# Performance work log

Hardware: AMD Instinct MI355X
Metric: run time of the kernel (lower is better)

## Reference

```python
import jax, jax.numpy as jnp
import numpy as np

K = 20
EPS = 1e-5


def knn_idx(x, k):
    # x: (B, N, C) -> (B, N, k) indices of k nearest neighbors (incl. self)
    xx = jnp.sum(x * x, axis=-1, keepdims=True)           # (B,N,1)
    inner = -2.0 * jnp.einsum('bnc,bmc->bnm', x, x)        # (B,N,N)
    pd = -xx - inner - jnp.swapaxes(xx, 1, 2)              # negative sq dist
    _, idx = jax.lax.top_k(pd, k)                          # (B,N,k)
    return idx


def get_graph_feature(x, k=K):
    B, N, C = x.shape
    idx = knn_idx(x, k)                                    # (B,N,k)
    # gather neighbor features per batch
    feature = jax.vmap(lambda xb, ib: xb[ib])(x, idx)      # (B,N,k,C)
    xe = jnp.broadcast_to(x[:, :, None, :], (B, N, k, C))  # (B,N,k,C)
    f = jnp.concatenate([feature - xe, xe], axis=3)        # (B,N,k,2C)
    return jnp.transpose(f, (0, 3, 1, 2))                  # (B,2C,N,k)


def conv1x1(x, W, b):
    # x: (B,Cin,N,k), W: (Cout,Cin)
    return jnp.einsum('bcnk,oc->bonk', x, W) + b[None, :, None, None]


def batchnorm(x, gamma, beta):
    # training-mode BN over (B,N,k) per channel, biased variance (torch default)
    mean = jnp.mean(x, axis=(0, 2, 3), keepdims=True)
    var = jnp.var(x, axis=(0, 2, 3), keepdims=True)
    xhat = (x - mean) * jax.lax.rsqrt(var + EPS)
    return xhat * gamma[None, :, None, None] + beta[None, :, None, None]


def setup_inputs() -> dict:
    key = jax.random.key(0)
    ks = jax.random.split(key, 10)
    B, N, C = 4, 4096, 3
    x = jax.random.normal(ks[0], (B, N, C), dtype=jnp.float32)
    W1 = jax.random.normal(ks[1], (64, 2 * C), dtype=jnp.float32) * 0.1
    b1 = jnp.zeros((64,), jnp.float32)
    g1 = jnp.ones((64,), jnp.float32)
    be1 = jnp.zeros((64,), jnp.float32)
    W2 = jax.random.normal(ks[2], (128, 64), dtype=jnp.float32) * 0.1
    b2 = jnp.zeros((128,), jnp.float32)
    g2 = jnp.ones((128,), jnp.float32)
    be2 = jnp.zeros((128,), jnp.float32)
    W3 = jax.random.normal(ks[3], (128, 128), dtype=jnp.float32) * 0.1
    b3 = jnp.zeros((128,), jnp.float32)
    g3 = jnp.ones((128,), jnp.float32)
    be3 = jnp.zeros((128,), jnp.float32)
    return {"x": x, "W1": W1, "b1": b1, "g1": g1, "be1": be1,
            "W2": W2, "b2": b2, "g2": g2, "be2": be2,
            "W3": W3, "b3": b3, "g3": g3, "be3": be3}


def reference(x, W1, b1, g1, be1, W2, b2, g2, be2, W3, b3, g3, be3):
    f = get_graph_feature(x, K)                  # (B,6,N,k)
    h = jax.nn.relu(batchnorm(conv1x1(f, W1, b1), g1, be1))
    h = jax.nn.relu(batchnorm(conv1x1(h, W2, b2), g2, be2))
    h = batchnorm(conv1x1(h, W3, b3), g3, be3)
    return jnp.max(h, axis=-1)                   # (B,128,N)
```

## Files before the change

kernel.cpp:

```cpp
#include <hip/hip_runtime.h>


typedef __attribute__((ext_vector_type(8)))  short short8;
typedef __attribute__((ext_vector_type(4)))  float floatx4;

#define BATCH 4
#define NPTS  4096
#define KNN   20
#define BN_   (BATCH*NPTS)
#define CNT   (BATCH*NPTS*KNN)

__device__ __forceinline__ unsigned short f2bf(float f) {
  unsigned u = __float_as_uint(f);
  unsigned r = u + 0x7FFFu + ((u >> 16) & 1u);
  return (unsigned short)(r >> 16);
}

__device__ __forceinline__ unsigned cvtpk(float lo, float hi) {
  unsigned r;
  asm("v_cvt_pk_bf16_f32 %0, %1, %2" : "=v"(r) : "v"(lo), "v"(hi));
  return r;
}

union PK8 { unsigned u4[4]; short8 s; };

__device__ __forceinline__ void store4bf_relu(unsigned short* dst, floatx4 v) {
  unsigned lo = cvtpk(fmaxf(v[0],0.f), fmaxf(v[1],0.f));
  unsigned hi = cvtpk(fmaxf(v[2],0.f), fmaxf(v[3],0.f));
  *(uint2*)dst = make_uint2(lo, hi);
}

__device__ __forceinline__ unsigned mono(float f) {
  unsigned u = __float_as_uint(f);
  return u ^ ((unsigned)((int)u >> 31) | 0x80000000u);
}

__device__ __forceinline__ void bn_affine(float gsum, float gsq, float gamma,
                                          float beta, float& s, float& sh) {
  const float inv = 1.0f / (float)CNT;
  float mean = gsum * inv;
  float var  = gsq * inv - mean * mean;
  s  = gamma * rsqrtf(var + 1e-5f);
  sh = beta - mean * s;
}

__global__ void pf_prep(const float* __restrict__ x, float4* __restrict__ xp,
                        float* __restrict__ stats,
                        const float* __restrict__ W2, const float* __restrict__ W3,
                        unsigned short* __restrict__ w2p,
                        unsigned short* __restrict__ w3p) {
  int pt = blockIdx.x * 256 + threadIdx.x;
  float x0 = x[pt*3+0], x1 = x[pt*3+1], x2 = x[pt*3+2];
  float xx = x0*x0 + x1*x1 + x2*x2;
  xp[pt] = make_float4(x0, x1, x2, xx);
  if (blockIdx.x == 0)
    for (int i = threadIdx.x; i < 640; i += 256) stats[i] = 0.0f;
  if (blockIdx.x == 1) {
    for (int i = threadIdx.x; i < 128*64;  i += 256) w2p[i] = f2bf(W2[i]);
    for (int i = threadIdx.x; i < 128*128; i += 256) w3p[i] = f2bf(W3[i]);
  }
}

__device__ __forceinline__ float sort_take20th(float v, int lane) {
  #pragma unroll
  for (int k = 2; k <= 64; k <<= 1) {
    #pragma unroll
    for (int j = k >> 1; j >= 1; j >>= 1) {
      float o = __shfl_xor(v, j);
      bool keepmax = (((lane & j) == 0) == ((lane & k) == 0));
      v = keepmax ? fmaxf(v, o) : fminf(v, o);
    }
  }
  return __shfl(v, 19);
}

__device__ __forceinline__ unsigned long long sort64_desc(unsigned long long v,
                                                          int lane) {
  #pragma unroll
  for (int k = 2; k <= 64; k <<= 1) {
    #pragma unroll
    for (int j = k >> 1; j >= 1; j >>= 1) {
      unsigned long long o = __shfl_xor(v, j);
      bool keepmax = (((lane & j) == 0) == ((lane & k) == 0));
      unsigned long long hi = v > o ? v : o;
      unsigned long long lo = v > o ? o : v;
      v = keepmax ? hi : lo;
    }
  }
  return v;
}

__global__ __launch_bounds__(256) void pf_knn(const float4* __restrict__ xp,
                                              int* __restrict__ idxb) {
  __shared__ unsigned long long lst[16][128];
  __shared__ int lcnt[16];
  const int tid  = threadIdx.x;
  const int lane = tid & 63;
  const int w    = tid >> 6;
  const int b    = blockIdx.x >> 8;
  const int nb   = (blockIdx.x & 255) * 16 + w * 4;
  const float4* xb = xp + b * NPTS;

  float4 q0 = xb[nb], q1 = xb[nb+1], q2 = xb[nb+2], q3 = xb[nb+3];

  float mx0=-3.0e38f, mx1=-3.0e38f, mx2=-3.0e38f, mx3=-3.0e38f;
  for (int j0 = 0; j0 < NPTS; j0 += 64) {
    float4 c = xb[j0 + lane];
    float d0 = fmaf(q0.x,c.x, fmaf(q0.y,c.y, q0.z*c.z));
    float d1 = fmaf(q1.x,c.x, fmaf(q1.y,c.y, q1.z*c.z));
    float d2 = fmaf(q2.x,c.x, fmaf(q2.y,c.y, q2.z*c.z));
    float d3 = fmaf(q3.x,c.x, fmaf(q3.y,c.y, q3.z*c.z));
    mx0 = fmaxf(mx0, fmaf(2.f,d0,-q0.w) - c.w);
    mx1 = fmaxf(mx1, fmaf(2.f,d1,-q1.w) - c.w);
    mx2 = fmaxf(mx2, fmaf(2.f,d2,-q2.w) - c.w);
    mx3 = fmaxf(mx3, fmaf(2.f,d3,-q3.w) - c.w);
  }
  float T0 = sort_take20th(mx0, lane);
  float T1 = sort_take20th(mx1, lane);
  float T2 = sort_take20th(mx2, lane);
  float T3 = sort_take20th(mx3, lane);

  if (lane < 4) lcnt[w*4 + lane] = 0;
  __syncthreads();

  for (int j0 = 0; j0 < NPTS; j0 += 64) {
    float4 c = xb[j0 + lane];
    float d0 = fmaf(q0.x,c.x, fmaf(q0.y,c.y, q0.z*c.z));
    float d1 = fmaf(q1.x,c.x, fmaf(q1.y,c.y, q1.z*c.z));
    float d2 = fmaf(q2.x,c.x, fmaf(q2.y,c.y, q2.z*c.z));
    float d3 = fmaf(q3.x,c.x, fmaf(q3.y,c.y, q3.z*c.z));
    float p0 = fmaf(2.f,d0,-q0.w) - c.w;
    float p1 = fmaf(2.f,d1,-q1.w) - c.w;
    float p2 = fmaf(2.f,d2,-q2.w) - c.w;
    float p3 = fmaf(2.f,d3,-q3.w) - c.w;
    unsigned long long keybase = (unsigned long long)(4095 - (j0 + lane));
    if (p0 >= T0) {
      int o = atomicAdd(&lcnt[w*4+0], 1);
      if (o < 128) lst[w*4+0][o] = ((unsigned long long)mono(p0) << 32) | keybase;
    }
    if (p1 >= T1) {
      int o = atomicAdd(&lcnt[w*4+1], 1);
      if (o < 128) lst[w*4+1][o] = ((unsigned long long)mono(p1) << 32) | keybase;
    }
    if (p2 >= T2) {
      int o = atomicAdd(&lcnt[w*4+2], 1);
      if (o < 128) lst[w*4+2][o] = ((unsigned long long)mono(p2) << 32) | keybase;
    }
    if (p3 >= T3) {
      int o = atomicAdd(&lcnt[w*4+3], 1);
      if (o < 128) lst[w*4+3][o] = ((unsigned long long)mono(p3) << 32) | keybase;
    }
  }

  #pragma unroll 1
  for (int i = 0; i < 4; ++i) {
    const int li = w*4 + i;
    const int cn = lcnt[li];
    const int outbase = (b * NPTS + nb + i) * KNN;
    if (cn <= 64) {
      unsigned long long v = (lane < cn) ? lst[li][lane] : 0ull;
      v = sort64_desc(v, lane);
      if (lane < KNN) idxb[outbase + lane] = 4095 - (int)(v & 0xFFFFFFFFull);
    } else if (cn <= 128) {
      unsigned long long e0 = lst[li][lane];
      unsigned long long e1 = (lane + 64 < cn) ? lst[li][lane + 64] : 0ull;
      #pragma unroll 1
      for (int r = 0; r < KNN; ++r) {
        unsigned long long m = e0 > e1 ? e0 : e1;
        #pragma unroll
        for (int o = 32; o; o >>= 1) {
          unsigned long long t = __shfl_xor(m, o);
          m = t > m ? t : m;
        }
        if (lane == 0) idxb[outbase + r] = 4095 - (int)(m & 0xFFFFFFFFull);
        if (e0 == m) e0 = 0ull; else if (e1 == m) e1 = 0ull;
      }
    } else {
      const float4 qq = (i == 0) ? q0 : (i == 1) ? q1 : (i == 2) ? q2 : q3;
      unsigned long long prev = ~0ull;
      #pragma unroll 1
      for (int r = 0; r < KNN; ++r) {
        unsigned long long best = 0ull;
        for (int j0 = 0; j0 < NPTS; j0 += 64) {
          float4 c = xb[j0 + lane];
          float dd = fmaf(qq.x,c.x, fmaf(qq.y,c.y, qq.z*c.z));
          float pd = fmaf(2.f,dd,-qq.w) - c.w;
          unsigned long long key = ((unsigned long long)mono(pd) << 32) |
                                   (unsigned long long)(4095 - (j0 + lane));
          if (key < prev && key > best) best = key;
        }
        #pragma unroll
        for (int o = 32; o; o >>= 1) {
          unsigned long long t = __shfl_xor(best, o);
          best = t > best ? t : best;
        }
        if (lane == 0) idxb[outbase + r] = 4095 - (int)(best & 0xFFFFFFFFull);
        prev = best;
      }
    }
  }
}

__global__ __launch_bounds__(256) void pf_mom(
    const float4* __restrict__ xp, const int* __restrict__ idxb,
    float* __restrict__ gm) {
  __shared__ float WM[4][27];
  const int tid = threadIdx.x, lane = tid & 63, w = tid >> 6;
  const int pt = blockIdx.x * 256 + tid;
  const float4 xi = xp[pt];
  const int ib = (pt >> 12) << 12;

  int idx[KNN];
  const int4* ip = (const int4*)(idxb + pt*KNN);
  #pragma unroll
  for (int q = 0; q < 5; ++q) {
    int4 v = ip[q];
    idx[q*4+0]=v.x; idx[q*4+1]=v.y; idx[q*4+2]=v.z; idx[q*4+3]=v.w;
  }
  float sj0=0,sj1=0,sj2=0, p0=0,p1=0,p2=0,p3=0,p4=0,p5=0;
  #pragma unroll
  for (int kk = 0; kk < KNN; ++kk) {
    float4 xj = xp[ib + idx[kk]];
    sj0 += xj.x; sj1 += xj.y; sj2 += xj.z;
    p0 = fmaf(xj.x,xj.x,p0); p1 = fmaf(xj.x,xj.y,p1); p2 = fmaf(xj.x,xj.z,p2);
    p3 = fmaf(xj.y,xj.y,p3); p4 = fmaf(xj.y,xj.z,p4); p5 = fmaf(xj.z,xj.z,p5);
  }
  float m[27];
  m[0]=sj0; m[1]=sj1; m[2]=sj2;
  m[3]=20.f*xi.x; m[4]=20.f*xi.y; m[5]=20.f*xi.z;
  m[6]=p0; m[7]=p1; m[8]=p2; m[9]=p3; m[10]=p4; m[11]=p5;
  m[12]=20.f*xi.x*xi.x; m[13]=20.f*xi.x*xi.y; m[14]=20.f*xi.x*xi.z;
  m[15]=20.f*xi.y*xi.y; m[16]=20.f*xi.y*xi.z; m[17]=20.f*xi.z*xi.z;
  m[18]=sj0*xi.x; m[19]=sj0*xi.y; m[20]=sj0*xi.z;
  m[21]=sj1*xi.x; m[22]=sj1*xi.y; m[23]=sj1*xi.z;
  m[24]=sj2*xi.x; m[25]=sj2*xi.y; m[26]=sj2*xi.z;
  #pragma unroll
  for (int c = 0; c < 27; ++c) {
    float v = m[c];
    #pragma unroll
    for (int o = 32; o; o >>= 1) v += __shfl_xor(v, o);
    m[c] = v;
  }
  if (lane == 0)
    #pragma unroll
    for (int c = 0; c < 27; ++c) WM[w][c] = m[c];
  __syncthreads();
  if (tid < 27) atomicAdd(&gm[tid], WM[0][tid]+WM[1][tid]+WM[2][tid]+WM[3][tid]);
}

__global__ void pf_affine1(const float* __restrict__ gm,
                           const float* __restrict__ W1,
                           const float* __restrict__ g1,
                           const float* __restrict__ be1,
                           unsigned short* __restrict__ w1s,
                           float* __restrict__ sh1e) {
  int c = threadIdx.x;
  if (c >= 64) return;
  const float* wr = W1 + c*6;
  const float wa[3] = {wr[0], wr[1], wr[2]};
  const float wb[3] = {wr[3], wr[4], wr[5]};
  const int si0[9] = {0,1,2, 1,3,4, 2,4,5};
  float syf = 0.f, sy2 = 0.f;
  #pragma unroll
  for (int a = 0; a < 3; ++a)
    syf += wa[a]*(gm[a] - gm[3+a]) + wb[a]*gm[3+a];
  #pragma unroll
  for (int a = 0; a < 3; ++a)
    #pragma unroll
    for (int bq = 0; bq < 3; ++bq) {
      int k = a*3 + bq, kt = bq*3 + a;
      float pjj = gm[6 + si0[k]], pii = gm[12 + si0[k]];
      float cc = gm[18 + k], ct = gm[18 + kt];
      float uu = pjj - cc - ct + pii;
      float uv = cc - pii;
      sy2 += wa[a]*wa[bq]*uu + 2.f*wa[a]*wb[bq]*uv + wb[a]*wb[bq]*pii;
    }
  const float inv = 1.0f / (float)CNT;
  float mean = syf * inv;
  float var  = sy2 * inv - mean * mean;
  float s  = g1[c] * rsqrtf(var + 1e-5f);
  sh1e[c]  = be1[c] - mean * s;
  unsigned short* o = w1s + c*8;
  o[0]=f2bf(s*wa[0]); o[1]=f2bf(s*wa[1]); o[2]=f2bf(s*wa[2]);
  o[3]=f2bf(s*wb[0]); o[4]=f2bf(s*wb[1]); o[5]=f2bf(s*wb[2]);
  o[6]=0; o[7]=0;
}

__global__ void pf_affine2(const float* __restrict__ gs2,
                           const float* __restrict__ gq2,
                           const float* __restrict__ W2,
                           const float* __restrict__ g2,
                           const float* __restrict__ be2,
                           unsigned short* __restrict__ w2s,
                           float* __restrict__ shm2) {
  int c = threadIdx.x;
  if (c >= 128) return;
  float s, sh; bn_affine(gs2[c], gq2[c], g2[c], be2[c], s, sh);
  shm2[c] = sh;
  const float* wr = W2 + c*64;
  unsigned short* o = w2s + c*64;
  for (int j = 0; j < 64; ++j) o[j] = f2bf(s * wr[j]);
}

__global__ __launch_bounds__(256, 4) void pf_stats2(
    const float4* __restrict__ xp, const int* __restrict__ idxb,
    const unsigned short* __restrict__ w1s, const float* __restrict__ sh1e,
    const unsigned short* __restrict__ w2p,
    float* __restrict__ gs2, float* __restrict__ gq2) {
  __shared__ __align__(16) short8 AF[KNN][16];
  __shared__ __align__(16) unsigned short H1[2][16][72];
  __shared__ float SS[128], SQ[128];

  const int tid = threadIdx.x;
  const int lane = tid & 63, ww = tid >> 6;
  const int l15 = lane & 15, quad = lane >> 4;
  const int pt0 = blockIdx.x * 16;

  if (tid < 128) { SS[tid] = 0.f; SQ[tid] = 0.f; }

  for (int u = tid; u < 16*KNN; u += 256) {
    int kk = u >> 4, pp = u & 15;
    int pt = pt0 + pp;
    float4 xi = xp[pt];
    float4 xj = xp[((pt >> 12) << 12) + idxb[pt*KNN + kk]];
    PK8 U;
    U.u4[0] = cvtpk(xj.x-xi.x, xj.y-xi.y);
    U.u4[1] = cvtpk(xj.z-xi.z, xi.x);
    U.u4[2] = cvtpk(xi.y, xi.z);
    U.u4[3] = 0;
    AF[kk][pp] = U.s;
  }

  short8 w1f = *(const short8*)(w1s + (16*ww + l15)*8);
  floatx4 sh1v;
  #pragma unroll
  for (int r = 0; r < 4; ++r) sh1v[r] = sh1e[16*ww + 4*quad + r];

  short8 w2f[2][2];
  #pragma unroll
  for (int ks = 0; ks < 2; ++ks)
    #pragma unroll
    for (int t = 0; t < 2; ++t)
      w2f[ks][t] = *(const short8*)(w2p + (32*ww + 16*t + l15)*64 + 32*ks + quad*8);

  float sum[2][4] = {{0,0,0,0},{0,0,0,0}}, sq[2][4] = {{0,0,0,0},{0,0,0,0}};
  const short8 z8 = {0,0,0,0,0,0,0,0};
  __syncthreads();

  #pragma unroll 1
  for (int kk = 0; kk < KNN; ++kk) {
    short8 a0 = z8;
    if (quad == 0) a0 = AF[kk][l15];
    floatx4 c0 = sh1v;
    c0 = __builtin_amdgcn_mfma_f32_16x16x32_bf16(w1f, a0, c0, 0,0,0);
    store4bf_relu(&H1[kk & 1][l15][16*ww + 4*quad], c0);
    __syncthreads();
    floatx4 acc2[2] = {{0,0,0,0},{0,0,0,0}};
    #pragma unroll
    for (int ks = 0; ks < 2; ++ks) {
      short8 a = *(const short8*)&H1[kk & 1][l15][ks*32 + quad*8];
      #pragma unroll
      for (int t = 0; t < 2; ++t)
        acc2[t] = __builtin_amdgcn_mfma_f32_16x16x32_bf16(w2f[ks][t], a, acc2[t], 0,0,0);
    }
    #pragma unroll
    for (int t = 0; t < 2; ++t)
      #pragma unroll
      for (int r = 0; r < 4; ++r) {
        float v = acc2[t][r];
        sum[t][r] += v; sq[t][r] = fmaf(v, v, sq[t][r]);
      }
  }
  #pragma unroll
  for (int t = 0; t < 2; ++t)
    #pragma unroll
    for (int r = 0; r < 4; ++r) {
      float s = sum[t][r], z = sq[t][r];
      s += __shfl_xor(s, 1); z += __shfl_xor(z, 1);
      s += __shfl_xor(s, 2); z += __shfl_xor(z, 2);
      s += __shfl_xor(s, 4); z += __shfl_xor(z, 4);
      s += __shfl_xor(s, 8); z += __shfl_xor(z, 8);
      if (l15 == 0) {
        int ch = 32*ww + 16*t + 4*quad + r;
        atomicAdd(&SS[ch], s); atomicAdd(&SQ[ch], z);
      }
    }
  __syncthreads();
  if (tid < 128) { atomicAdd(&gs2[tid], SS[tid]); atomicAdd(&gq2[tid], SQ[tid]); }
}

__global__ __launch_bounds__(256, 4) void pf_main(
    const float4* __restrict__ xp, const int* __restrict__ idxb,
    const unsigned short* __restrict__ w1s, const float* __restrict__ sh1e,
    const unsigned short* __restrict__ w2s, const float* __restrict__ shm2,
    const unsigned short* __restrict__ w3p,
    float* __restrict__ gs3, float* __restrict__ gq3,
    float* __restrict__ maxv) {
  __shared__ __align__(16) short8 AF[KNN][16];
  __shared__ __align__(16) unsigned short H1[16][72];
  __shared__ __align__(16) unsigned short H2[16][136];
  __shared__ float SS[128], SQ[128];

  const int tid = threadIdx.x;
  const int lane = tid & 63, ww = tid >> 6;
  const int l15 = lane & 15, quad = lane >> 4;
  const int pt0 = blockIdx.x * 16;

  if (tid < 128) { SS[tid] = 0.f; SQ[tid] = 0.f; }

  for (int u = tid; u < 16*KNN; u += 256) {
    int kk = u >> 4, pp = u & 15;
    int pt = pt0 + pp;
    float4 xi = xp[pt];
    float4 xj = xp[((pt >> 12) << 12) + idxb[pt*KNN + kk]];
    PK8 U;
    U.u4[0] = cvtpk(xj.x-xi.x, xj.y-xi.y);
    U.u4[1] = cvtpk(xj.z-xi.z, xi.x);
    U.u4[2] = cvtpk(xi.y, xi.z);
    U.u4[3] = 0;
    AF[kk][pp] = U.s;
  }

  short8 w1f = *(const short8*)(w1s + (16*ww + l15)*8);
  floatx4 sh1v;
  #pragma unroll
  for (int r = 0; r < 4; ++r) sh1v[r] = sh1e[16*ww + 4*quad + r];
  short8 w2f[2][2];
  #pragma unroll
  for (int ks = 0; ks < 2; ++ks)
    #pragma unroll
    for (int t = 0; t < 2; ++t)
      w2f[ks][t] = *(const short8*)(w2s + (32*ww + 16*t + l15)*64 + 32*ks + quad*8);
  floatx4 sh2v[2];
  #pragma unroll
  for (int t = 0; t < 2; ++t)
    #pragma unroll
    for (int r = 0; r < 4; ++r)
      sh2v[t][r] = shm2[32*ww + 16*t + 4*quad + r];
  short8 w3f[4][2];
  #pragma unroll
  for (int ks = 0; ks < 4; ++ks)
    #pragma unroll
    for (int t = 0; t < 2; ++t)
      w3f[ks][t] = *(const short8*)(w3p + (32*ww + 16*t + l15)*128 + 32*ks + quad*8);

  float sum[2][4] = {{0,0,0,0},{0,0,0,0}}, sq[2][4] = {{0,0,0,0},{0,0,0,0}};
  float mx[2][4];
  #pragma unroll
  for (int t = 0; t < 2; ++t)
    #pragma unroll
    for (int r = 0; r < 4; ++r) mx[t][r] = -3.0e38f;

  const short8 z8 = {0,0,0,0,0,0,0,0};
  __syncthreads();

  #pragma unroll 1
  for (int kk = 0; kk < KNN; ++kk) {
    short8 a0 = z8;
    if (quad == 0) a0 = AF[kk][l15];
    floatx4 acc1 = sh1v;
    acc1 = __builtin_amdgcn_mfma_f32_16x16x32_bf16(w1f, a0, acc1, 0,0,0);
    store4bf_relu(&H1[l15][16*ww + 4*quad], acc1);
    __syncthreads();
    floatx4 acc2[2] = {sh2v[0], sh2v[1]};
    #pragma unroll
    for (int ks = 0; ks < 2; ++ks) {
      short8 a = *(const short8*)&H1[l15][ks*32 + quad*8];
      #pragma unroll
      for (int t = 0; t < 2; ++t)
        acc2[t] = __builtin_amdgcn_mfma_f32_16x16x32_bf16(w2f[ks][t], a, acc2[t], 0,0,0);
    }
    #pragma unroll
    for (int t = 0; t < 2; ++t)
      store4bf_relu(&H2[l15][32*ww + 16*t + 4*quad], acc2[t]);
    __syncthreads();
    floatx4 acc3[2] = {{0,0,0,0},{0,0,0,0}};
    #pragma unroll
    for (int ks = 0; ks < 4; ++ks) {
      short8 a = *(const short8*)&H2[l15][ks*32 + quad*8];
      #pragma unroll
      for (int t = 0; t < 2; ++t)
        acc3[t] = __builtin_amdgcn_mfma_f32_16x16x32_bf16(w3f[ks][t], a, acc3[t], 0,0,0);
    }
    #pragma unroll
    for (int t = 0; t < 2; ++t)
      #pragma unroll
      for (int r = 0; r < 4; ++r) {
        float v = acc3[t][r];
        sum[t][r] += v; sq[t][r] = fmaf(v, v, sq[t][r]);
        mx[t][r] = fmaxf(mx[t][r], v);
      }
  }

  #pragma unroll
  for (int t = 0; t < 2; ++t) {
    int ch0 = 32*ww + 16*t + 4*quad;
    float4 o = make_float4(mx[t][0], mx[t][1], mx[t][2], mx[t][3]);
    *(float4*)&maxv[(size_t)(pt0 + l15)*128 + ch0] = o;
  }
  #pragma unroll
  for (int t = 0; t < 2; ++t)
    #pragma unroll
    for (int r = 0; r < 4; ++r) {
      float s = sum[t][r], z = sq[t][r];
      s += __shfl_xor(s, 1); z += __shfl_xor(z, 1);
      s += __shfl_xor(s, 2); z += __shfl_xor(z, 2);
      s += __shfl_xor(s, 4); z += __shfl_xor(z, 4);
      s += __shfl_xor(s, 8); z += __shfl_xor(z, 8);
      if (l15 == 0) {
        int ch = 32*ww + 16*t + 4*quad + r;
        atomicAdd(&SS[ch], s); atomicAdd(&SQ[ch], z);
      }
    }
  __syncthreads();
  if (tid < 128) { atomicAdd(&gs3[tid], SS[tid]); atomicAdd(&gq3[tid], SQ[tid]); }
}

__global__ __launch_bounds__(256) void pf_out(
    const float* __restrict__ maxv,
    const float* __restrict__ gs3, const float* __restrict__ gq3,
    const float* __restrict__ g3, const float* __restrict__ be3,
    float* __restrict__ out) {
  __shared__ float T[128][17];
  __shared__ float SC[128], SH[128];
  const int tid = threadIdx.x;
  const int b  = blockIdx.x >> 8;
  const int n0 = (blockIdx.x & 255) * 16;
  if (tid < 128) {
    float s, sh; bn_affine(gs3[tid], gq3[tid], g3[tid], be3[tid], s, sh);
    SC[tid] = s; SH[tid] = sh;
  }
  __syncthreads();
  const float4* mv4 = (const float4*)maxv;
  #pragma unroll
  for (int r = 0; r < 2; ++r) {
    int fid = r * 256 + tid;
    int nl = fid >> 5, c4 = fid & 31;
    float4 v = mv4[(size_t)(b*NPTS + n0 + nl)*32 + c4];
    int c = c4 * 4;
    T[c+0][nl] = fmaf(SC[c+0], v.x, SH[c+0]);
    T[c+1][nl] = fmaf(SC[c+1], v.y, SH[c+1]);
    T[c+2][nl] = fmaf(SC[c+2], v.z, SH[c+2]);
    T[c+3][nl] = fmaf(SC[c+3], v.w, SH[c+3]);
  }
  __syncthreads();
  #pragma unroll
  for (int r = 0; r < 2; ++r) {
    int fid = r * 256 + tid;
    int c = fid >> 2, nq = fid & 3;
    float4 o;
    o.x = T[c][nq*4+0]; o.y = T[c][nq*4+1];
    o.z = T[c][nq*4+2]; o.w = T[c][nq*4+3];
    *(float4*)(out + (size_t)b*128*NPTS + (size_t)c*NPTS + n0 + nq*4) = o;
  }
}

extern "C" void kernel_launch(void* const* d_in, const int* in_sizes, int n_in,
                              void* d_out, int out_size, void* d_ws, size_t ws_size,
                              hipStream_t stream) {
  const float* x   = (const float*)d_in[0];
  const float* W1  = (const float*)d_in[1];
  const float* g1  = (const float*)d_in[3];
  const float* be1 = (const float*)d_in[4];
  const float* W2  = (const float*)d_in[5];
  const float* g2  = (const float*)d_in[7];
  const float* be2 = (const float*)d_in[8];
  const float* W3  = (const float*)d_in[9];
  const float* g3  = (const float*)d_in[11];
  const float* be3 = (const float*)d_in[12];
  float* out = (float*)d_out;

  char* p = (char*)d_ws;
  float4* xp  = (float4*)p;            p += (size_t)BN_ * 16;
  int*    idxb= (int*)p;               p += (size_t)BN_ * KNN * 4;
  float*  stats = (float*)p;           p += 640 * 4;
  float*  aff   = (float*)p;           p += 256 * 4;
  unsigned short* w1s = (unsigned short*)p; p += 64 * 8 * 2;
  unsigned short* w2p = (unsigned short*)p; p += 128 * 64 * 2;
  unsigned short* w2s = (unsigned short*)p; p += 128 * 64 * 2;
  unsigned short* w3p = (unsigned short*)p; p += 128 * 128 * 2;
  float*  maxv  = (float*)p;

  float *gm  = stats;
  float *gs2 = stats + 128, *gq2 = stats + 256;
  float *gs3 = stats + 384, *gq3 = stats + 512;
  float *sh1e = aff, *shm2 = aff + 64;

  pf_prep   <<<64,   256, 0, stream>>>(x, xp, stats, W2, W3, w2p, w3p);
  pf_knn    <<<1024, 256, 0, stream>>>(xp, idxb);
  pf_mom    <<<64,   256, 0, stream>>>(xp, idxb, gm);
  pf_affine1<<<1,    64,  0, stream>>>(gm, W1, g1, be1, w1s, sh1e);
  pf_stats2 <<<1024, 256, 0, stream>>>(xp, idxb, w1s, sh1e, w2p, gs2, gq2);
  pf_affine2<<<1,    128, 0, stream>>>(gs2, gq2, W2, g2, be2, w2s, shm2);
  pf_main   <<<1024, 256, 0, stream>>>(xp, idxb, w1s, sh1e, w2s, shm2,
                                       w3p, gs3, gq3, maxv);
  pf_out    <<<1024, 256, 0, stream>>>(maxv, gs3, gq3, g3, be3, out);
}
```

Baseline: 225.8 us.

## Software-pipeline per-neighbor MLP layers across iterations with double-buffered LDS

The per-neighbor loops in the stats kernel and the main kernel are restructured so that layer 1 for neighbor k, layer 2 for k-1 and layer 3 for k-2 all run in the same iteration. H1 and H2 become double buffers, so each iteration needs only one barrier instead of one per layer. The aim is to cut barrier stalls and give the scheduler independent MFMA work to overlap. In exchange the loops run one or two extra iterations, LDS use grows slightly and the guarded stages add branching.

```diff
diff --git a/kernel.cpp b/kernel.cpp
--- a/kernel.cpp
+++ b/kernel.cpp
@@ -348,28 +348,32 @@
   __syncthreads();
 
   #pragma unroll 1
-  for (int kk = 0; kk < KNN; ++kk) {
-    short8 a0 = z8;
-    if (quad == 0) a0 = AF[kk][l15];
-    floatx4 c0 = sh1v;
-    c0 = __builtin_amdgcn_mfma_f32_16x16x32_bf16(w1f, a0, c0, 0,0,0);
-    store4bf_relu(&H1[kk & 1][l15][16*ww + 4*quad], c0);
-    __syncthreads();
-    floatx4 acc2[2] = {{0,0,0,0},{0,0,0,0}};
-    #pragma unroll
-    for (int ks = 0; ks < 2; ++ks) {
-      short8 a = *(const short8*)&H1[kk & 1][l15][ks*32 + quad*8];
+  for (int k = 0; k < KNN + 1; ++k) {
+    if (k >= 1) {
+      floatx4 acc2[2] = {{0,0,0,0},{0,0,0,0}};
+      #pragma unroll
+      for (int ks = 0; ks < 2; ++ks) {
+        short8 a = *(const short8*)&H1[(k-1) & 1][l15][ks*32 + quad*8];
+        #pragma unroll
+        for (int t = 0; t < 2; ++t)
+          acc2[t] = __builtin_amdgcn_mfma_f32_16x16x32_bf16(w2f[ks][t], a, acc2[t], 0,0,0);
+      }
       #pragma unroll
       for (int t = 0; t < 2; ++t)
-        acc2[t] = __builtin_amdgcn_mfma_f32_16x16x32_bf16(w2f[ks][t], a, acc2[t], 0,0,0);
-    }
-    #pragma unroll
-    for (int t = 0; t < 2; ++t)
-      #pragma unroll
-      for (int r = 0; r < 4; ++r) {
-        float v = acc2[t][r];
-        sum[t][r] += v; sq[t][r] = fmaf(v, v, sq[t][r]);
-      }
+        #pragma unroll
+        for (int r = 0; r < 4; ++r) {
+          float v = acc2[t][r];
+          sum[t][r] += v; sq[t][r] = fmaf(v, v, sq[t][r]);
+        }
+    }
+    if (k < KNN) {
+      short8 a0 = z8;
+      if (quad == 0) a0 = AF[k][l15];
+      floatx4 c0 = sh1v;
+      c0 = __builtin_amdgcn_mfma_f32_16x16x32_bf16(w1f, a0, c0, 0,0,0);
+      store4bf_relu(&H1[k & 1][l15][16*ww + 4*quad], c0);
+    }
+    __syncthreads();
   }
   #pragma unroll
   for (int t = 0; t < 2; ++t)
@@ -397,8 +401,8 @@
     float* __restrict__ gs3, float* __restrict__ gq3,
     float* __restrict__ maxv) {
   __shared__ __align__(16) short8 AF[KNN][16];
-  __shared__ __align__(16) unsigned short H1[16][72];
-  __shared__ __align__(16) unsigned short H2[16][136];
+  __shared__ __align__(16) unsigned short H1[2][16][72];
+  __shared__ __align__(16) unsigned short H2[2][16][136];
   __shared__ float SS[128], SQ[128];
 
   const int tid = threadIdx.x;
@@ -455,41 +459,46 @@
   __syncthreads();
 
   #pragma unroll 1
-  for (int kk = 0; kk < KNN; ++kk) {
-    short8 a0 = z8;
-    if (quad == 0) a0 = AF[kk][l15];
-    floatx4 acc1 = sh1v;
-    acc1 = __builtin_amdgcn_mfma_f32_16x16x32_bf16(w1f, a0, acc1, 0,0,0);
-    store4bf_relu(&H1[l15][16*ww + 4*quad], acc1);
-    __syncthreads();
-    floatx4 acc2[2] = {sh2v[0], sh2v[1]};
-    #pragma unroll
-    for (int ks = 0; ks < 2; ++ks) {
-      short8 a = *(const short8*)&H1[l15][ks*32 + quad*8];
+  for (int k = 0; k < KNN + 2; ++k) {
+    if (k >= 2) {
+      floatx4 acc3[2] = {{0,0,0,0},{0,0,0,0}};
+      #pragma unroll
+      for (int ks = 0; ks < 4; ++ks) {
+        short8 a = *(const short8*)&H2[k & 1][l15][ks*32 + quad*8];
+        #pragma unroll
+        for (int t = 0; t < 2; ++t)
+          acc3[t] = __builtin_amdgcn_mfma_f32_16x16x32_bf16(w3f[ks][t], a, acc3[t], 0,0,0);
+      }
       #pragma unroll
       for (int t = 0; t < 2; ++t)
-        acc2[t] = __builtin_amdgcn_mfma_f32_16x16x32_bf16(w2f[ks][t], a, acc2[t], 0,0,0);
-    }
-    #pragma unroll
-    for (int t = 0; t < 2; ++t)
-      store4bf_relu(&H2[l15][32*ww + 16*t + 4*quad], acc2[t]);
-    __syncthreads();
-    floatx4 acc3[2] = {{0,0,0,0},{0,0,0,0}};
-    #pragma unroll
-    for (int ks = 0; ks < 4; ++ks) {
-      short8 a = *(const short8*)&H2[l15][ks*32 + quad*8];
+        #pragma unroll
+        for (int r = 0; r < 4; ++r) {
+          float v = acc3[t][r];
+          sum[t][r] += v; sq[t][r] = fmaf(v, v, sq[t][r]);
+          mx[t][r] = fmaxf(mx[t][r], v);
+        }
+    }
+    if (k >= 1 && k < KNN + 1) {
+      floatx4 acc2[2] = {sh2v[0], sh2v[1]};
+      #pragma unroll
+      for (int ks = 0; ks < 2; ++ks) {
+        short8 a = *(const short8*)&H1[(k-1) & 1][l15][ks*32 + quad*8];
+        #pragma unroll
+        for (int t = 0; t < 2; ++t)
+          acc2[t] = __builtin_amdgcn_mfma_f32_16x16x32_bf16(w2f[ks][t], a, acc2[t], 0,0,0);
+      }
       #pragma unroll
       for (int t = 0; t < 2; ++t)
-        acc3[t] = __builtin_amdgcn_mfma_f32_16x16x32_bf16(w3f[ks][t], a, acc3[t], 0,0,0);
-    }
-    #pragma unroll
-    for (int t = 0; t < 2; ++t)
-      #pragma unroll
-      for (int r = 0; r < 4; ++r) {
-        float v = acc3[t][r];
-        sum[t][r] += v; sq[t][r] = fmaf(v, v, sq[t][r]);
-        mx[t][r] = fmaxf(mx[t][r], v);
-      }
+        store4bf_relu(&H2[(k-1) & 1][l15][32*ww + 16*t + 4*quad], acc2[t]);
+    }
+    if (k < KNN) {
+      short8 a0 = z8;
+      if (quad == 0) a0 = AF[k][l15];
+      floatx4 acc1 = sh1v;
+      acc1 = __builtin_amdgcn_mfma_f32_16x16x32_bf16(w1f, a0, acc1, 0,0,0);
+      store4bf_relu(&H1[k & 1][l15][16*ww + 4*quad], acc1);
+    }
+    __syncthreads();
   }
 
   #pragma unroll
```

After: 228.8 us. No clear change (+1.3%).
